# Performance work log

Hardware: AMD Instinct MI355X
Metric: run time of the kernel (lower is better)

Reference implementation:

```python
import jax, jax.numpy as jnp
import numpy as np

NC = 80          # num classes
REG_MAX = 16     # DFL bins
STRIDES = (8, 16, 32)
FEAT_HW = ((80, 80), (40, 40), (20, 20))
MAX_DET = 100
CONF_THRES = 0.25
IOU_THRES = 0.45
PRE_TOPK = 1000  # pre-NMS candidate count (EfficientNMS-style preselection)


def setup_inputs() -> dict:
    key = jax.random.key(0)
    k1, k2, k3 = jax.random.split(key, 3)
    B = 32
    no = 4 * REG_MAX + NC  # 144
    return {
        "p3": jax.random.normal(k1, (B, no, 80, 80), dtype=jnp.float32),
        "p4": jax.random.normal(k2, (B, no, 40, 40), dtype=jnp.float32),
        "p5": jax.random.normal(k3, (B, no, 20, 20), dtype=jnp.float32),
    }


def _make_anchors():
    # grid_cell_offset = 0.5, matching ultralytics make_anchors
    pts, strs = [], []
    for (h, w), s in zip(FEAT_HW, STRIDES):
        sx = jnp.arange(w, dtype=jnp.float32) + 0.5
        sy = jnp.arange(h, dtype=jnp.float32) + 0.5
        yy, xx = jnp.meshgrid(sy, sx, indexing="ij")
        pts.append(jnp.stack([xx.ravel(), yy.ravel()], axis=-1))  # [h*w, 2]
        strs.append(jnp.full((h * w, 1), float(s), dtype=jnp.float32))
    return jnp.concatenate(pts, 0), jnp.concatenate(strs, 0)  # [A,2], [A,1]


def _pairwise_iou(b):
    # b: [K, 4] xyxy
    area = (b[:, 2] - b[:, 0]) * (b[:, 3] - b[:, 1])
    lt = jnp.maximum(b[:, None, :2], b[None, :, :2])
    rb = jnp.minimum(b[:, None, 2:], b[None, :, 2:])
    wh = jnp.clip(rb - lt, 0.0)
    inter = wh[..., 0] * wh[..., 1]
    return inter / (area[:, None] + area[None, :] - inter + 1e-7)


def _nms_single(bxyxy, conf):
    # Greedy class-agnostic NMS over PRE_TOPK score-sorted boxes.
    K = bxyxy.shape[0]
    iou = _pairwise_iou(bxyxy)  # [K, K]
    idx = jnp.arange(K)

    def step(suppressed, xs):
        i, row = xs
        keep = jnp.logical_and(jnp.logical_not(suppressed[i]), conf[i] > 0.0)
        suppressed = jnp.logical_or(suppressed, keep & (row > IOU_THRES) & (idx > i))
        return suppressed, keep

    _, keeps = jax.lax.scan(step, jnp.zeros(K, dtype=bool), (idx, iou))
    return keeps  # [K] bool


def reference(p3, p4, p5):
    feats = [p3, p4, p5]
    B = p3.shape[0]
    no = 4 * REG_MAX + NC
    # concat across scales: [B, no, A]
    x_cat = jnp.concatenate([f.reshape(B, no, -1) for f in feats], axis=2)
    box, cls = x_cat[:, : 4 * REG_MAX], x_cat[:, 4 * REG_MAX:]

    anchors, strd = _make_anchors()  # [A,2], [A,1]
    A = box.shape[-1]

    # DFL: softmax over reg_max bins, expectation with arange weights
    prob = jax.nn.softmax(box.reshape(B, 4, REG_MAX, A), axis=2)
    dist = jnp.einsum("bkra,r->bka", prob, jnp.arange(REG_MAX, dtype=jnp.float32))

    # dist2bbox (xywh) then scale by stride
    anc = anchors.T  # [2, A]
    lt, rb = dist[:, :2], dist[:, 2:]
    x1y1 = anc - lt
    x2y2 = anc + rb
    dbox = jnp.concatenate([(x1y1 + x2y2) * 0.5, x2y2 - x1y1], axis=1) * strd.T  # [B,4,A]

    boxes = dbox.transpose(0, 2, 1)                       # [B, A, 4] xywh
    scores = jax.nn.sigmoid(cls).transpose(0, 2, 1)       # [B, A, NC] (score_activation=1)

    # class-agnostic: best class per box
    conf = scores.max(-1)                                 # [B, A]
    cls_id = jnp.argmax(scores, -1)                       # [B, A]
    conf_m = jnp.where(conf > CONF_THRES, conf, -1.0)

    topv, topi = jax.lax.top_k(conf_m, PRE_TOPK)          # [B, K]
    bsel = jnp.take_along_axis(boxes, topi[..., None], axis=1)  # [B, K, 4]
    cx, cy, w, h = bsel[..., 0], bsel[..., 1], bsel[..., 2], bsel[..., 3]
    bxyxy = jnp.stack([cx - w * 0.5, cy - h * 0.5, cx + w * 0.5, cy + h * 0.5], -1)

    keeps = jax.vmap(_nms_single)(bxyxy, topv)            # [B, K]
    kept_scores = jnp.where(keeps, topv, -1.0)
    dv, di = jax.lax.top_k(kept_scores, MAX_DET)          # [B, MAX_DET]
    valid = dv > 0.0

    det_scores = jnp.where(valid, dv, 0.0)
    det_boxes = jnp.take_along_axis(bxyxy, di[..., None], axis=1) * valid[..., None]
    sel_cls = jnp.take_along_axis(jnp.take_along_axis(cls_id, topi, 1), di, 1)
    det_classes = jnp.where(valid, sel_cls, 0).astype(jnp.int32)
    num_dets = valid.sum(-1, keepdims=True).astype(jnp.int32)
    return num_dets, det_boxes, det_scores, det_classes
```

## Files before the change

kernel.cpp:

```cpp
#include <hip/hip_runtime.h>
#include <math.h>

#define NCLS 80
#define NA 8400
#define NB 32
#define NO 144
#define PRE_TOPK 1000
#define MAX_DET 100

template<int HW, int WDIM, int S>
__device__ __forceinline__ void decode_store(
    const float* __restrict__ src, int g, int aoff,
    float* __restrict__ conf, int* __restrict__ clsid, float* __restrict__ box)
{
    int b = g / HW;
    int pos = g - b * HW;
    float ax = (float)(pos % WDIM) + 0.5f;
    float ay = (float)(pos / WDIM) + 0.5f;
    const float* base = src + (size_t)b * (NO * HW) + pos;

    float vd[64];
    #pragma unroll
    for (int i = 0; i < 64; ++i) vd[i] = base[(size_t)i * HW];

    float vc[80];
    #pragma unroll
    for (int c = 0; c < 80; ++c) vc[c] = base[(size_t)(64 + c) * HW];

    float m0 = vc[0];  int i0 = 0;
    float m1 = vc[20]; int i1 = 20;
    float m2 = vc[40]; int i2 = 40;
    float m3 = vc[60]; int i3 = 60;
    #pragma unroll
    for (int c = 1; c < 20; ++c) {
        if (vc[c]      > m0) { m0 = vc[c];      i0 = c;      }
        if (vc[20 + c] > m1) { m1 = vc[20 + c]; i1 = 20 + c; }
        if (vc[40 + c] > m2) { m2 = vc[40 + c]; i2 = 40 + c; }
        if (vc[60 + c] > m3) { m3 = vc[60 + c]; i3 = 60 + c; }
    }
    float m = m0; int bid = i0;
    if (m1 > m) { m = m1; bid = i1; }
    if (m2 > m) { m = m2; bid = i2; }
    if (m3 > m) { m = m3; bid = i3; }
    float conf_v = 1.0f / (1.0f + __expf(-m));

    float dist[4];
    #pragma unroll
    for (int s4 = 0; s4 < 4; ++s4) {
        float mm = vd[s4 * 16];
        #pragma unroll
        for (int r = 1; r < 16; ++r) mm = fmaxf(mm, vd[s4 * 16 + r]);
        float e[16]; float sum = 0.f;
        #pragma unroll
        for (int r = 0; r < 16; ++r) { e[r] = __expf(vd[s4 * 16 + r] - mm); sum += e[r]; }
        float inv = 1.0f / sum;
        float d = 0.f;
        #pragma unroll
        for (int r = 1; r < 16; ++r) d += (e[r] * inv) * (float)r;
        dist[s4] = d;
    }

    float x1 = ax - dist[0], y1 = ay - dist[1];
    float x2 = ax + dist[2], y2 = ay + dist[3];
    float cx = ((x1 + x2) * 0.5f) * (float)S;
    float cy = ((y1 + y2) * 0.5f) * (float)S;
    float w  = (x2 - x1) * (float)S;
    float h  = (y2 - y1) * (float)S;

    size_t gid = (size_t)b * NA + aoff + pos;
    conf[gid]  = conf_v;
    clsid[gid] = bid;
    *(float4*)(box + gid * 4) = make_float4(cx, cy, w, h);
}

__global__ __launch_bounds__(256) void k_decode(
    const float* __restrict__ p3, const float* __restrict__ p4, const float* __restrict__ p5,
    float* __restrict__ conf, int* __restrict__ clsid, float* __restrict__ box)
{
    int blk = blockIdx.x;
    int t = threadIdx.x;
    if (blk < 800) {
        int g = blk * 256 + t;
        decode_store<6400, 80, 8>(p3, g, 0, conf, clsid, box);
    } else if (blk < 1000) {
        int g = (blk - 800) * 256 + t;
        decode_store<1600, 40, 16>(p4, g, 6400, conf, clsid, box);
    } else {
        int g = (blk - 1000) * 256 + t;
        decode_store<400, 20, 32>(p5, g, 8000, conf, clsid, box);
    }
}

__device__ __forceinline__ uint32_t ord_bits(float f) {
    uint32_t u = __float_as_uint(f);
    return (u & 0x80000000u) ? ~u : (u | 0x80000000u);
}

__global__ __launch_bounds__(1024) void k_topk(
    const float* __restrict__ conf, const float* __restrict__ box, const int* __restrict__ clsid,
    float* __restrict__ topv, float* __restrict__ bxyxy, int* __restrict__ topcls)
{
    int b = blockIdx.x;
    int t = threadIdx.x;

    __shared__ uint32_t ob[NA];
    __shared__ uint32_t hist[256];
    __shared__ uint64_t sbuf[1024];
    __shared__ uint64_t s_prefix;
    __shared__ int s_k;
    __shared__ int s_cnt;

    const float* cf = conf + (size_t)b * NA;
    for (int i = t; i < NA; i += 1024) {
        float c = cf[i];
        float cm = (c > 0.25f) ? c : -1.0f;
        ob[i] = ord_bits(cm);
    }
    if (t == 0) { s_prefix = 0; s_k = PRE_TOPK; s_cnt = 0; }
    sbuf[t] = 0;
    __syncthreads();

    for (int pass = 0; pass < 8; ++pass) {
        int shift = 56 - 8 * pass;
        if (t < 256) hist[t] = 0;
        __syncthreads();
        uint64_t prefix = s_prefix;
        int k = s_k;
        for (int i = t; i < NA; i += 1024) {
            uint64_t key = ((uint64_t)ob[i] << 32) | (uint64_t)(0xFFFFFFFFu - (uint32_t)i);
            bool match = (pass == 0) || (((key ^ prefix) >> (64 - 8 * pass)) == 0);
            if (match) atomicAdd(&hist[(uint32_t)(key >> shift) & 255u], 1u);
        }
        __syncthreads();
        if (t < 64) {
            uint32_t h0 = hist[4 * t + 0], h1 = hist[4 * t + 1];
            uint32_t h2 = hist[4 * t + 2], h3 = hist[4 * t + 3];
            uint32_t part = h0 + h1 + h2 + h3;
            uint32_t s = part;
            #pragma unroll
            for (int off = 1; off < 64; off <<= 1) {
                uint32_t v = __shfl_down(s, off);
                if (t + off < 64) s += v;
            }
            uint32_t cb3 = s - part;
            uint32_t cb2 = cb3 + h3;
            uint32_t cb1 = cb2 + h2;
            uint32_t cb0 = cb1 + h1;
            uint32_t ku = (uint32_t)k;
            if (cb3 < ku && ku <= cb3 + h3) { s_k = k - (int)cb3; s_prefix = prefix | ((uint64_t)(uint32_t)(4 * t + 3) << shift); }
            if (cb2 < ku && ku <= cb2 + h2) { s_k = k - (int)cb2; s_prefix = prefix | ((uint64_t)(uint32_t)(4 * t + 2) << shift); }
            if (cb1 < ku && ku <= cb1 + h1) { s_k = k - (int)cb1; s_prefix = prefix | ((uint64_t)(uint32_t)(4 * t + 1) << shift); }
            if (cb0 < ku && ku <= cb0 + h0) { s_k = k - (int)cb0; s_prefix = prefix | ((uint64_t)(uint32_t)(4 * t + 0) << shift); }
        }
        __syncthreads();
    }

    uint64_t kstar = s_prefix;
    for (int i = t; i < NA; i += 1024) {
        uint64_t key = ((uint64_t)ob[i] << 32) | (uint64_t)(0xFFFFFFFFu - (uint32_t)i);
        if (key >= kstar) {
            int p = atomicAdd(&s_cnt, 1);
            if (p < 1024) sbuf[p] = key;
        }
    }
    __syncthreads();

    for (int k = 2; k <= 1024; k <<= 1) {
        for (int j = k >> 1; j > 0; j >>= 1) {
            int ixj = t ^ j;
            if (ixj > t) {
                uint64_t A = sbuf[t], Bv = sbuf[ixj];
                bool descBlock = ((t & k) == 0);
                bool sw = descBlock ? (A < Bv) : (A > Bv);
                if (sw) { sbuf[t] = Bv; sbuf[ixj] = A; }
            }
            __syncthreads();
        }
    }

    if (t < PRE_TOPK) {
        uint64_t key = sbuf[t];
        uint32_t u = (uint32_t)(key >> 32);
        uint32_t fb = (u & 0x80000000u) ? (u ^ 0x80000000u) : ~u;
        float val = __uint_as_float(fb);
        int idx = (int)(0xFFFFFFFFu - (uint32_t)(key & 0xFFFFFFFFull));
        size_t g = (size_t)b * NA + idx;
        float cx = box[g * 4 + 0], cy = box[g * 4 + 1];
        float w  = box[g * 4 + 2], h  = box[g * 4 + 3];
        size_t o = (size_t)b * PRE_TOPK + t;
        topv[o] = val;
        bxyxy[o * 4 + 0] = cx - w * 0.5f;
        bxyxy[o * 4 + 1] = cy - h * 0.5f;
        bxyxy[o * 4 + 2] = cx + w * 0.5f;
        bxyxy[o * 4 + 3] = cy + h * 0.5f;
        topcls[o] = clsid[g];
    }
}

__global__ __launch_bounds__(256) void k_iou(
    const float* __restrict__ bxyxy, unsigned long long* __restrict__ mask)
{
    __shared__ float4 boxes[PRE_TOPK];
    int b = blockIdx.y;
    int t = threadIdx.x;
    const float4* bp = (const float4*)(bxyxy + (size_t)b * PRE_TOPK * 4);
    for (int i = t; i < PRE_TOPK; i += 256) boxes[i] = bp[i];
    __syncthreads();

    int r_local = t >> 4, w = t & 15;
    int row = blockIdx.x * 16 + r_local;
    if (row >= PRE_TOPK) return;

    float4 bi = boxes[row];
    float area_i = (bi.z - bi.x) * (bi.w - bi.y);
    unsigned long long bits = 0;
    int j0 = w * 64;
    #pragma unroll 4
    for (int jj = 0; jj < 64; ++jj) {
        int j = j0 + jj;
        if (j >= PRE_TOPK) break;
        if (j <= row) continue;
        float4 bj = boxes[j];
        float lx = fmaxf(bi.x, bj.x), ly = fmaxf(bi.y, bj.y);
        float rx = fminf(bi.z, bj.z), ry = fminf(bi.w, bj.w);
        float iw = fmaxf(rx - lx, 0.f), ih = fmaxf(ry - ly, 0.f);
        float inter = iw * ih;
        float area_j = (bj.z - bj.x) * (bj.w - bj.y);
        float iou = inter / (area_i + area_j - inter + 1e-7f);
        if (iou > 0.45f) bits |= (1ull << jj);
    }
    mask[((size_t)b * PRE_TOPK + row) * 16 + w] = bits;
}

#define CHUNK 125
__global__ __launch_bounds__(256) void k_nms(
    const unsigned long long* __restrict__ mask, const float* __restrict__ topv,
    const float* __restrict__ bxyxy, const int* __restrict__ topcls,
    float* __restrict__ out)
{
    int b = blockIdx.x;
    int t = threadIdx.x;

    __shared__ unsigned long long mrows[CHUNK * 16];
    __shared__ float sv[PRE_TOPK];
    __shared__ int kept[MAX_DET];
    __shared__ unsigned long long s_supp[16];
    __shared__ int s_cnt;
    __shared__ int s_done;

    for (int i = t; i < PRE_TOPK; i += 256) sv[i] = topv[(size_t)b * PRE_TOPK + i];
    if (t == 0) { s_cnt = 0; s_done = 0; }
    if (t < 16) s_supp[t] = 0;
    __syncthreads();

    for (int c = 0; c < 8; ++c) {
        int base = c * CHUNK;
        for (int i = t; i < CHUNK * 16; i += 256) {
            int row = base + (i >> 4);
            if (row < PRE_TOPK)
                mrows[i] = mask[((size_t)b * PRE_TOPK + row) * 16 + (i & 15)];
        }
        __syncthreads();
        if (t < 64) {
            unsigned long long supp = (t < 16) ? s_supp[t] : 0ull;
            int cnt = s_cnt;
            int end = base + CHUNK;
            for (int i = base; i < end; ++i) {
                int wsel = i >> 6, bit = i & 63;
                int sbit = (int)((supp >> bit) & 1ull);
                sbit = __shfl(sbit, wsel);
                bool keep = (!sbit) && (sv[i] > 0.0f);
                if (keep) {
                    if (t < 16) supp |= mrows[(i - base) * 16 + t];
                    if (t == 0 && cnt < MAX_DET) kept[cnt] = i;
                    ++cnt;
                }
            }
            if (t < 16) s_supp[t] = supp;
            if (t == 0) { s_cnt = cnt; if (cnt >= MAX_DET) s_done = 1; }
        }
        __syncthreads();
        if (s_done) break;
    }

    int cnt = s_cnt; if (cnt > MAX_DET) cnt = MAX_DET;
    if (t == 0) out[b] = (float)cnt;
    if (t < MAX_DET) {
        bool valid = t < cnt;
        float bx0 = 0.f, bx1 = 0.f, bx2 = 0.f, bx3 = 0.f, sc = 0.f, cl = 0.f;
        if (valid) {
            int p = kept[t];
            size_t o = (size_t)b * PRE_TOPK + p;
            sc = sv[p];
            bx0 = bxyxy[o * 4 + 0];
            bx1 = bxyxy[o * 4 + 1];
            bx2 = bxyxy[o * 4 + 2];
            bx3 = bxyxy[o * 4 + 3];
            cl = (float)topcls[o];
        }
        size_t db = 32 + ((size_t)b * MAX_DET + t) * 4;
        out[db + 0] = bx0; out[db + 1] = bx1; out[db + 2] = bx2; out[db + 3] = bx3;
        out[32 + 12800 + (size_t)b * MAX_DET + t] = sc;
        out[32 + 16000 + (size_t)b * MAX_DET + t] = cl;
    }
}

extern "C" void kernel_launch(void* const* d_in, const int* in_sizes, int n_in,
                              void* d_out, int out_size, void* d_ws, size_t ws_size,
                              hipStream_t stream)
{
    const float* p3 = (const float*)d_in[0];
    const float* p4 = (const float*)d_in[1];
    const float* p5 = (const float*)d_in[2];
    float* out = (float*)d_out;

    char* ws = (char*)d_ws;
    size_t off_mask = 0;
    size_t off_conf = off_mask + (size_t)NB * PRE_TOPK * 16 * 8;
    size_t off_cls  = off_conf + (size_t)NB * NA * 4;
    size_t off_box  = off_cls  + (size_t)NB * NA * 4;
    size_t off_topv = off_box  + (size_t)NB * NA * 4 * 4;
    size_t off_topc = off_topv + (size_t)NB * PRE_TOPK * 4;
    size_t off_bx   = off_topc + (size_t)NB * PRE_TOPK * 4;

    unsigned long long* mask = (unsigned long long*)(ws + off_mask);
    float* conf   = (float*)(ws + off_conf);
    int*   clsid  = (int*)(ws + off_cls);
    float* box    = (float*)(ws + off_box);
    float* topv   = (float*)(ws + off_topv);
    int*   topcls = (int*)(ws + off_topc);
    float* bxyxy  = (float*)(ws + off_bx);

    k_decode<<<1050, 256, 0, stream>>>(p3, p4, p5, conf, clsid, box);
    k_topk<<<NB, 1024, 0, stream>>>(conf, box, clsid, topv, bxyxy, topcls);
    k_iou<<<dim3((PRE_TOPK + 15) / 16, NB), 256, 0, stream>>>(bxyxy, mask);
    k_nms<<<NB, 256, 0, stream>>>(mask, topv, bxyxy, topcls, out);
}
```

Baseline: 158.9 us.

## Restructure decode loads, warp-aggregate histogram, pad IOU smem, rewrite NMS scan

The decode kernel now streams the DFL and class channels in smaller groups instead of holding all 144 values in registers, which lowers register pressure. The top-k histogram groups equal digits within a wavefront via ballots so each group issues one atomic, reducing LDS atomic contention. IOU box staging pads shared memory to avoid bank conflicts. NMS now loads the whole mask into LDS and picks the next kept box with a bitmask-plus-ctz search instead of a per-candidate serial loop, and several box accesses are vectorized to float4.

```diff
diff --git a/kernel.cpp b/kernel.cpp
--- a/kernel.cpp
+++ b/kernel.cpp
@@ -19,46 +19,37 @@
     float ay = (float)(pos / WDIM) + 0.5f;
     const float* base = src + (size_t)b * (NO * HW) + pos;
 
-    float vd[64];
-    #pragma unroll
-    for (int i = 0; i < 64; ++i) vd[i] = base[(size_t)i * HW];
-
-    float vc[80];
-    #pragma unroll
-    for (int c = 0; c < 80; ++c) vc[c] = base[(size_t)(64 + c) * HW];
-
-    float m0 = vc[0];  int i0 = 0;
-    float m1 = vc[20]; int i1 = 20;
-    float m2 = vc[40]; int i2 = 40;
-    float m3 = vc[60]; int i3 = 60;
-    #pragma unroll
-    for (int c = 1; c < 20; ++c) {
-        if (vc[c]      > m0) { m0 = vc[c];      i0 = c;      }
-        if (vc[20 + c] > m1) { m1 = vc[20 + c]; i1 = 20 + c; }
-        if (vc[40 + c] > m2) { m2 = vc[40 + c]; i2 = 40 + c; }
-        if (vc[60 + c] > m3) { m3 = vc[60 + c]; i3 = 60 + c; }
-    }
-    float m = m0; int bid = i0;
-    if (m1 > m) { m = m1; bid = i1; }
-    if (m2 > m) { m = m2; bid = i2; }
-    if (m3 > m) { m = m3; bid = i3; }
-    float conf_v = 1.0f / (1.0f + __expf(-m));
-
     float dist[4];
     #pragma unroll
     for (int s4 = 0; s4 < 4; ++s4) {
-        float mm = vd[s4 * 16];
-        #pragma unroll
-        for (int r = 1; r < 16; ++r) mm = fmaxf(mm, vd[s4 * 16 + r]);
-        float e[16]; float sum = 0.f;
-        #pragma unroll
-        for (int r = 0; r < 16; ++r) { e[r] = __expf(vd[s4 * 16 + r] - mm); sum += e[r]; }
+        float v[16];
+        #pragma unroll
+        for (int r = 0; r < 16; ++r) v[r] = base[(size_t)(s4 * 16 + r) * HW];
+        float mm = v[0];
+        #pragma unroll
+        for (int r = 1; r < 16; ++r) mm = fmaxf(mm, v[r]);
+        float sum = 0.f;
+        #pragma unroll
+        for (int r = 0; r < 16; ++r) { v[r] = __expf(v[r] - mm); sum += v[r]; }
         float inv = 1.0f / sum;
         float d = 0.f;
         #pragma unroll
-        for (int r = 1; r < 16; ++r) d += (e[r] * inv) * (float)r;
+        for (int r = 1; r < 16; ++r) d += (v[r] * inv) * (float)r;
         dist[s4] = d;
     }
+
+    float best = -INFINITY; int bid = 0;
+    #pragma unroll
+    for (int ch = 0; ch < 4; ++ch) {
+        float vc[20];
+        #pragma unroll
+        for (int c = 0; c < 20; ++c) vc[c] = base[(size_t)(64 + ch * 20 + c) * HW];
+        float m = vc[0]; int ii = 0;
+        #pragma unroll
+        for (int c = 1; c < 20; ++c) if (vc[c] > m) { m = vc[c]; ii = c; }
+        if (m > best) { best = m; bid = ch * 20 + ii; }
+    }
+    float conf_v = 1.0f / (1.0f + __expf(-best));
 
     float x1 = ax - dist[0], y1 = ay - dist[1];
     float x2 = ax + dist[2], y2 = ay + dist[3];
@@ -96,12 +87,13 @@
     return (u & 0x80000000u) ? ~u : (u | 0x80000000u);
 }
 
-__global__ __launch_bounds__(1024) void k_topk(
+__global__ __launch_bounds__(1024) void k_select(
     const float* __restrict__ conf, const float* __restrict__ box, const int* __restrict__ clsid,
     float* __restrict__ topv, float* __restrict__ bxyxy, int* __restrict__ topcls)
 {
     int b = blockIdx.x;
     int t = threadIdx.x;
+    int lane = t & 63;
 
     __shared__ uint32_t ob[NA];
     __shared__ uint32_t hist[256];
@@ -129,7 +121,17 @@
         for (int i = t; i < NA; i += 1024) {
             uint64_t key = ((uint64_t)ob[i] << 32) | (uint64_t)(0xFFFFFFFFu - (uint32_t)i);
             bool match = (pass == 0) || (((key ^ prefix) >> (64 - 8 * pass)) == 0);
-            if (match) atomicAdd(&hist[(uint32_t)(key >> shift) & 255u], 1u);
+            uint32_t d = (uint32_t)(key >> shift) & 255u;
+            if (match) {
+                uint64_t m = __ballot(1);
+                #pragma unroll
+                for (int bb = 0; bb < 8; ++bb) {
+                    uint64_t bal = __ballot((d >> bb) & 1u);
+                    m &= ((d >> bb) & 1u) ? bal : ~bal;
+                }
+                if ((m & ((1ull << lane) - 1ull)) == 0ull)
+                    atomicAdd(&hist[d], (uint32_t)__popcll(m));
+            }
         }
         __syncthreads();
         if (t < 64) {
@@ -185,33 +187,33 @@
         float val = __uint_as_float(fb);
         int idx = (int)(0xFFFFFFFFu - (uint32_t)(key & 0xFFFFFFFFull));
         size_t g = (size_t)b * NA + idx;
-        float cx = box[g * 4 + 0], cy = box[g * 4 + 1];
-        float w  = box[g * 4 + 2], h  = box[g * 4 + 3];
+        float4 bx = *(const float4*)(box + g * 4);
+        float cx = bx.x, cy = bx.y, w = bx.z, h = bx.w;
         size_t o = (size_t)b * PRE_TOPK + t;
         topv[o] = val;
-        bxyxy[o * 4 + 0] = cx - w * 0.5f;
-        bxyxy[o * 4 + 1] = cy - h * 0.5f;
-        bxyxy[o * 4 + 2] = cx + w * 0.5f;
-        bxyxy[o * 4 + 3] = cy + h * 0.5f;
+        *(float4*)(bxyxy + o * 4) = make_float4(cx - w * 0.5f, cy - h * 0.5f,
+                                                cx + w * 0.5f, cy + h * 0.5f);
         topcls[o] = clsid[g];
     }
 }
+
+__device__ __forceinline__ int bslot(int j) { return j + (j >> 6); }
 
 __global__ __launch_bounds__(256) void k_iou(
     const float* __restrict__ bxyxy, unsigned long long* __restrict__ mask)
 {
-    __shared__ float4 boxes[PRE_TOPK];
+    __shared__ float4 boxes[PRE_TOPK + 16];
     int b = blockIdx.y;
     int t = threadIdx.x;
     const float4* bp = (const float4*)(bxyxy + (size_t)b * PRE_TOPK * 4);
-    for (int i = t; i < PRE_TOPK; i += 256) boxes[i] = bp[i];
+    for (int i = t; i < PRE_TOPK; i += 256) boxes[bslot(i)] = bp[i];
     __syncthreads();
 
     int r_local = t >> 4, w = t & 15;
     int row = blockIdx.x * 16 + r_local;
     if (row >= PRE_TOPK) return;
 
-    float4 bi = boxes[row];
+    float4 bi = boxes[bslot(row)];
     float area_i = (bi.z - bi.x) * (bi.w - bi.y);
     unsigned long long bits = 0;
     int j0 = w * 64;
@@ -220,7 +222,7 @@
         int j = j0 + jj;
         if (j >= PRE_TOPK) break;
         if (j <= row) continue;
-        float4 bj = boxes[j];
+        float4 bj = boxes[bslot(j)];
         float lx = fmaxf(bi.x, bj.x), ly = fmaxf(bi.y, bj.y);
         float rx = fminf(bi.z, bj.z), ry = fminf(bi.w, bj.w);
         float iw = fmaxf(rx - lx, 0.f), ih = fmaxf(ry - ly, 0.f);
@@ -232,8 +234,7 @@
     mask[((size_t)b * PRE_TOPK + row) * 16 + w] = bits;
 }
 
-#define CHUNK 125
-__global__ __launch_bounds__(256) void k_nms(
+__global__ __launch_bounds__(1024) void k_nms(
     const unsigned long long* __restrict__ mask, const float* __restrict__ topv,
     const float* __restrict__ bxyxy, const int* __restrict__ topcls,
     float* __restrict__ out)
@@ -241,47 +242,56 @@
     int b = blockIdx.x;
     int t = threadIdx.x;
 
-    __shared__ unsigned long long mrows[CHUNK * 16];
+    __shared__ __align__(16) unsigned long long smask[PRE_TOPK * 16];
     __shared__ float sv[PRE_TOPK];
+    __shared__ unsigned long long s_valid[16];
     __shared__ int kept[MAX_DET];
-    __shared__ unsigned long long s_supp[16];
     __shared__ int s_cnt;
-    __shared__ int s_done;
-
-    for (int i = t; i < PRE_TOPK; i += 256) sv[i] = topv[(size_t)b * PRE_TOPK + i];
-    if (t == 0) { s_cnt = 0; s_done = 0; }
-    if (t < 16) s_supp[t] = 0;
-    __syncthreads();
-
-    for (int c = 0; c < 8; ++c) {
-        int base = c * CHUNK;
-        for (int i = t; i < CHUNK * 16; i += 256) {
-            int row = base + (i >> 4);
-            if (row < PRE_TOPK)
-                mrows[i] = mask[((size_t)b * PRE_TOPK + row) * 16 + (i & 15)];
-        }
-        __syncthreads();
-        if (t < 64) {
-            unsigned long long supp = (t < 16) ? s_supp[t] : 0ull;
-            int cnt = s_cnt;
-            int end = base + CHUNK;
-            for (int i = base; i < end; ++i) {
-                int wsel = i >> 6, bit = i & 63;
-                int sbit = (int)((supp >> bit) & 1ull);
-                sbit = __shfl(sbit, wsel);
-                bool keep = (!sbit) && (sv[i] > 0.0f);
-                if (keep) {
-                    if (t < 16) supp |= mrows[(i - base) * 16 + t];
-                    if (t == 0 && cnt < MAX_DET) kept[cnt] = i;
-                    ++cnt;
-                }
+
+    for (int i = t; i < PRE_TOPK; i += 1024) sv[i] = topv[(size_t)b * PRE_TOPK + i];
+    {
+        const ulonglong2* src = (const ulonglong2*)(mask + (size_t)b * PRE_TOPK * 16);
+        ulonglong2* dst = (ulonglong2*)smask;
+        for (int i = t; i < PRE_TOPK * 8; i += 1024) dst[i] = src[i];
+    }
+    __syncthreads();
+
+    {
+        bool pred = (t < PRE_TOPK) && (sv[t] > 0.0f);
+        unsigned long long bal = __ballot(pred);
+        if ((t & 63) == 0) s_valid[t >> 6] = bal;
+    }
+    __syncthreads();
+
+    if (t < 64) {
+        int w = t;
+        unsigned long long supp = 0;
+        unsigned long long valid = (w < 16) ? s_valid[w] : 0ull;
+        int base = w * 64;
+        int cur = -1;
+        int cnt = 0;
+        while (cnt < MAX_DET) {
+            unsigned long long gt;
+            if (cur < base)            gt = ~0ull;
+            else if (cur - base >= 63) gt = 0ull;
+            else                       gt = (~0ull) << (cur - base + 1);
+            unsigned long long cand = valid & ~supp & gt;
+            int idx = cand ? (base + __builtin_ctzll(cand)) : 0x7FFFFFFF;
+            #pragma unroll
+            for (int off = 8; off >= 1; off >>= 1) {
+                int o = __shfl_xor(idx, off);
+                idx = (o < idx) ? o : idx;
             }
-            if (t < 16) s_supp[t] = supp;
-            if (t == 0) { s_cnt = cnt; if (cnt >= MAX_DET) s_done = 1; }
-        }
-        __syncthreads();
-        if (s_done) break;
-    }
+            int nxt = __shfl(idx, 0);
+            if (nxt == 0x7FFFFFFF) break;
+            if (t == 0) kept[cnt] = nxt;
+            ++cnt;
+            if (w < 16) supp |= smask[nxt * 16 + w];
+            cur = nxt;
+        }
+        if (t == 0) s_cnt = cnt;
+    }
+    __syncthreads();
 
     int cnt = s_cnt; if (cnt > MAX_DET) cnt = MAX_DET;
     if (t == 0) out[b] = (float)cnt;
@@ -291,11 +301,9 @@
         if (valid) {
             int p = kept[t];
             size_t o = (size_t)b * PRE_TOPK + p;
+            float4 bb = *(const float4*)(bxyxy + o * 4);
+            bx0 = bb.x; bx1 = bb.y; bx2 = bb.z; bx3 = bb.w;
             sc = sv[p];
-            bx0 = bxyxy[o * 4 + 0];
-            bx1 = bxyxy[o * 4 + 1];
-            bx2 = bxyxy[o * 4 + 2];
-            bx3 = bxyxy[o * 4 + 3];
             cl = (float)topcls[o];
         }
         size_t db = 32 + ((size_t)b * MAX_DET + t) * 4;
@@ -332,7 +340,7 @@
     float* bxyxy  = (float*)(ws + off_bx);
 
     k_decode<<<1050, 256, 0, stream>>>(p3, p4, p5, conf, clsid, box);
-    k_topk<<<NB, 1024, 0, stream>>>(conf, box, clsid, topv, bxyxy, topcls);
+    k_select<<<NB, 1024, 0, stream>>>(conf, box, clsid, topv, bxyxy, topcls);
     k_iou<<<dim3((PRE_TOPK + 15) / 16, NB), 256, 0, stream>>>(bxyxy, mask);
-    k_nms<<<NB, 256, 0, stream>>>(mask, topv, bxyxy, topcls, out);
-}
+    k_nms<<<NB, 1024, 0, stream>>>(mask, topv, bxyxy, topcls, out);
+}
```

Measured after the change: 144.2 us. 9.2% less time.
